# Optimization experiments

Measured on AMD Instinct MI355X. Metric: run time of the kernel, lower is better.

## Reference

```python
import jax, jax.numpy as jnp
import numpy as np

BS, N, HID = 16384, 16, 512  # batch, n coords (state dim = 2n), mlp hidden


def setup_inputs() -> dict:
    key = jax.random.key(0)
    ks = jax.random.split(key, 4)
    d = 2 * N
    x = jax.random.normal(ks[0], (BS, d), dtype=jnp.float32)
    # Lagrangian MLP: 2n -> HID -> HID -> 1 with softplus (smooth 2nd derivs)
    W1 = jax.random.normal(ks[1], (d, HID), dtype=jnp.float32) / np.sqrt(d)
    b1 = jnp.zeros((HID,), jnp.float32)
    W2 = jax.random.normal(ks[2], (HID, HID), dtype=jnp.float32) / np.sqrt(HID)
    b2 = jnp.zeros((HID,), jnp.float32)
    W3 = jax.random.normal(ks[3], (HID, 1), dtype=jnp.float32) / np.sqrt(HID)
    b3 = jnp.zeros((1,), jnp.float32)
    return {"x": x, "W1": W1, "b1": b1, "W2": W2, "b2": b2, "W3": W3, "b3": b3}


def reference(x, W1, b1, W2, b2, W3, b3):
    n = x.shape[1] // 2

    def lagrangian(qqd):  # qqd: [2n] -> scalar
        h = jax.nn.softplus(qqd @ W1 + b1)
        h = jax.nn.softplus(h @ W2 + b2)
        return jnp.sum(h @ W3 + b3)

    # batched first derivative (jacobian of scalar) and hessian; replaces the
    # per-sample python loop of torch.autograd.functional.jacobian/hessian
    jac = jax.vmap(jax.grad(lagrangian))(x)          # [bs, 2n]
    hess = jax.vmap(jax.hessian(lagrangian))(x)      # [bs, 2n, 2n]

    qd = x[:, n:]                                    # [bs, n]
    A = hess[:, n:, n:]                              # d2L/dqd dqd  [bs, n, n]
    B = hess[:, n:, :n]                              # d2L/dqd dq   [bs, n, n]
    rhs = jac[:, :n] - jnp.einsum('bij,bj->bi', B, qd)  # [bs, n]
    qdd = jnp.einsum('bij,bj->bi', jnp.linalg.pinv(A), rhs)  # [bs, n]
    return jnp.concatenate([qd, qdd], axis=1)        # [bs, 2n]
```

## Files before the change

### kernel.cpp

```cpp
#include <hip/hip_runtime.h>
#include <math.h>


#define NSWEEP 5
#define JAX_RCOND 1.9073486e-5

typedef unsigned int uint;
typedef unsigned short ushort;
typedef float f2 __attribute__((ext_vector_type(2)));
typedef float f4 __attribute__((ext_vector_type(4)));
typedef short bf16x8 __attribute__((ext_vector_type(8)));
typedef float f32x16 __attribute__((ext_vector_type(16)));
typedef uint uint2v __attribute__((ext_vector_type(2)));

#define OFF_R    0
#define R_FLOATS 6144
#define OFF_S1   (OFF_R + R_FLOATS)
#define OFF_H1   (OFF_S1+512)
#define OFF_G2   (OFF_H1+512)
#define OFF_D2   (OFF_G2+512)
#define OFF_U    (OFF_D2+512)
#define OFF_X    (OFF_U+512)
#define OFF_JAC  (OFF_X+32)
#define OFF_T1   (OFF_JAC+16)
#define OFF_T2   (OFF_T1+528)
#define OFF_AUG  (OFF_T2+528)
#define SMEM_FLOATS (OFF_AUG+272)
#define SMEM_BYTES  (SMEM_FLOATS*4)

#define SOLVE_WAVE_DBL 592
#define SOLVE_SMEM_BYTES (4*SOLVE_WAVE_DBL*8)

#define PACK_BYTES 524288

__device__ __forceinline__ ushort f2bf(float x) {
    uint u = __float_as_uint(x);
    return (ushort)((u + 0x7fffu + ((u >> 16) & 1u)) >> 16);
}
__device__ __forceinline__ float bf2f(ushort h) {
    return __uint_as_float(((uint)h) << 16);
}
__device__ __forceinline__ void split3(float x, ushort& h, ushort& m, ushort& l) {
    h = f2bf(x); float r1 = x - bf2f(h);
    m = f2bf(r1); float r2 = r1 - bf2f(m);
    l = f2bf(r2);
}

__device__ __forceinline__ void pairpq(int r, int m, int& p, int& q) {
    p = (m == 0) ? 0 : 1 + (m - 1 + r) % 15;
    q = 1 + (14 - m + r) % 15;
}

__device__ __forceinline__ void wave_fence() {
    __builtin_amdgcn_wave_barrier();
    __builtin_amdgcn_s_waitcnt(0);
    __builtin_amdgcn_wave_barrier();
}

__device__ __forceinline__ void jacobi_solve_wave(
    const float* __restrict__ gaug, double* __restrict__ ws,
    float* __restrict__ outp, int lane)
{
    double* Ad  = ws;
    double* Vd  = Ad + 272;
    double* c8  = Vd + 272;
    double* sn8 = c8 + 8;
    double* il  = sn8 + 8;
    double* yv  = il + 16;

    for (int idx = lane; idx < 272; idx += 64) {
        const int r = idx / 17, c = idx - r*17;
        double a = 0.0;
        if (c < 16) a = 0.5 * ((double)gaug[r*17 + c] + (double)gaug[c*17 + r]);
        Ad[idx] = a;
        Vd[idx] = (c < 16 && r == c) ? 1.0 : 0.0;
    }
    wave_fence();

    for (int sweep = 0; sweep < NSWEEP; ++sweep) {
        for (int rr = 0; rr < 15; ++rr) {
            if (lane < 8) {
                int p, q; pairpq(rr, lane, p, q);
                const double app = Ad[p*17 + p], aqq = Ad[q*17 + q], apq = Ad[p*17 + q];
                double cc = 1.0, ss = 0.0;
                if (apq != 0.0) {
                    const double tau = (aqq - app) / (2.0 * apq);
                    const double tt = ((tau >= 0.0) ? 1.0 : -1.0) / (fabs(tau) + sqrt(1.0 + tau*tau));
                    cc = 1.0 / sqrt(1.0 + tt*tt);
                    ss = tt * cc;
                }
                c8[lane] = cc; sn8[lane] = ss;
            }
            wave_fence();
            #pragma unroll
            for (int k = 0; k < 2; ++k) {
                const int id = lane + 64*k;
                const int m = id >> 4, j = id & 15;
                int p, q; pairpq(rr, m, p, q);
                const double cc = c8[m], ss = sn8[m];
                const double ap = Ad[p*17 + j], aq = Ad[q*17 + j];
                Ad[p*17 + j] = cc*ap - ss*aq;
                Ad[q*17 + j] = ss*ap + cc*aq;
            }
            #pragma unroll
            for (int k = 0; k < 2; ++k) {
                const int id = lane + 64*k;
                const int m = id >> 4, i = id & 15;
                int p, q; pairpq(rr, m, p, q);
                const double cc = c8[m], ss = sn8[m];
                const double vp = Vd[i*17 + p], vq = Vd[i*17 + q];
                Vd[i*17 + p] = cc*vp - ss*vq;
                Vd[i*17 + q] = ss*vp + cc*vq;
            }
            wave_fence();
            #pragma unroll
            for (int k = 0; k < 2; ++k) {
                const int id = lane + 64*k;
                const int m = id >> 4, i = id & 15;
                int p, q; pairpq(rr, m, p, q);
                const double cc = c8[m], ss = sn8[m];
                const double ap = Ad[i*17 + p], aq = Ad[i*17 + q];
                Ad[i*17 + p] = cc*ap - ss*aq;
                Ad[i*17 + q] = ss*ap + cc*aq;
            }
            wave_fence();
        }
    }

    if (lane == 0) {
        double mx = 0.0;
        #pragma unroll
        for (int i = 0; i < 16; ++i) mx = fmax(mx, fabs(Ad[i*17 + i]));
        const double cut = JAX_RCOND * mx;
        #pragma unroll
        for (int i = 0; i < 16; ++i) {
            const double l = Ad[i*17 + i];
            il[i] = (fabs(l) > cut) ? (1.0 / l) : 0.0;
        }
    }
    wave_fence();

    if (lane < 16) {
        double a = 0.0;
        #pragma unroll
        for (int r = 0; r < 16; ++r) a += Vd[r*17 + lane] * (double)gaug[r*17 + 16];
        yv[lane] = a;
    }
    wave_fence();

    if (lane < 16) {
        double a = 0.0;
        #pragma unroll
        for (int i = 0; i < 16; ++i) a += Vd[lane*17 + i] * (il[i] * yv[i]);
        outp[lane] = (float)a;
    }
}

extern "C" __global__ void w1_transpose(const float* __restrict__ W1,
                                        float* __restrict__ W1T) {
    const int t = blockIdx.x * 256 + threadIdx.x;
    W1T[t] = W1[(t & 31) * 512 + (t >> 5)];
}

extern "C" __global__ void w2_pack(const float* __restrict__ W2,
                                   uint* __restrict__ pHi,
                                   uint* __restrict__ pMid,
                                   uint* __restrict__ pLo) {
    const int tid = blockIdx.x * 256 + threadIdx.x;
    const int lane = tid & 63;
    const int k0 = ((tid >> 6) & 31) * 16 + (lane >> 5) * 8;
    const int n  = (tid >> 11) * 32 + (lane & 31);
    uint h[4], m[4], l[4];
    #pragma unroll
    for (int e2 = 0; e2 < 4; ++e2) {
        ushort h0, m0, l0, h1, m1, l1;
        split3(W2[(k0 + 2*e2    )*512 + n], h0, m0, l0);
        split3(W2[(k0 + 2*e2 + 1)*512 + n], h1, m1, l1);
        h[e2] = (uint)h0 | ((uint)h1 << 16);
        m[e2] = (uint)m0 | ((uint)m1 << 16);
        l[e2] = (uint)l0 | ((uint)l1 << 16);
    }
    #pragma unroll
    for (int e2 = 0; e2 < 4; ++e2) {
        pHi [tid*4 + e2] = h[e2];
        pMid[tid*4 + e2] = m[e2];
        pLo [tid*4 + e2] = l[e2];
    }
}

#define MFMA32(A, B, C) __builtin_amdgcn_mfma_f32_32x32x16_bf16((A), (B), (C), 0, 0, 0)

extern "C" __global__ __launch_bounds__(256, 4)
void lnn_kernel(const float* __restrict__ x,
                const float* __restrict__ W1,
                const float* __restrict__ W1T,
                const float* __restrict__ b1,
                const float* __restrict__ W2, const float* __restrict__ b2,
                const float* __restrict__ W3,
                float* __restrict__ out,
                float* __restrict__ aug_g,
                const uint* __restrict__ pHi,
                const uint* __restrict__ pMid,
                const uint* __restrict__ pLo,
                const int solveInMain)
{
    const int b = blockIdx.x;
    const int t = threadIdx.x;
    const int lane = t & 63;
    const int w = t >> 6;

    extern __shared__ float sm[];
    char*  A8    = (char*)sm;
    float* s_ws  = sm + OFF_R;
    char*  Mq8   = (char*)sm;
    float* s_s1  = sm + OFF_S1;
    float* s_h1  = sm + OFF_H1;
    float* s_g2  = sm + OFF_G2;
    float* s_d2  = sm + OFF_D2;
    float* s_u   = sm + OFF_U;
    float* s_x   = sm + OFF_X;
    float* s_jac = sm + OFF_JAC;
    float* s_T1  = sm + OFF_T1;
    float* s_T2  = sm + OFF_T2;
    float* s_aug = sm + OFF_AUG;

    if (t < 32) s_x[t] = x[b*32 + t];
    if (t < 16) out[b*32 + t] = x[b*32 + 16 + t];
    __syncthreads();

    #pragma unroll
    for (int rep = 0; rep < 2; ++rep) {
        const int j = t + rep*256;
        float z = b1[j];
        const f4* wt = (const f4*)(W1T + j*32);
        #pragma unroll
        for (int i4 = 0; i4 < 8; ++i4) {
            const f4 wv = wt[i4];
            z = fmaf(s_x[i4*4 + 0], wv.x, z);
            z = fmaf(s_x[i4*4 + 1], wv.y, z);
            z = fmaf(s_x[i4*4 + 2], wv.z, z);
            z = fmaf(s_x[i4*4 + 3], wv.w, z);
        }
        const float e = expf(-fabsf(z));
        const float s = (z >= 0.f) ? 1.f/(1.f+e) : e/(1.f+e);
        s_s1[j] = s;
        s_h1[j] = fmaxf(z, 0.f) + log1pf(e);
    }
    __syncthreads();

    {
        const int c = w*128 + lane*2;
        const f2 bz = *(const f2*)(b2 + c);
        float za0 = bz.x, za1 = bz.y;
        #pragma unroll 16
        for (int j = 0; j < 512; ++j) {
            const f2 wv = *(const f2*)(W2 + j*512 + c);
            const float h = s_h1[j];
            za0 = fmaf(h, wv.x, za0);
            za1 = fmaf(h, wv.y, za1);
        }
        const f2 w3v = *(const f2*)(W3 + c);
        const float e0 = expf(-fabsf(za0));
        const float sg0 = (za0 >= 0.f) ? 1.f/(1.f+e0) : e0/(1.f+e0);
        const float e1v = expf(-fabsf(za1));
        const float sg1 = (za1 >= 0.f) ? 1.f/(1.f+e1v) : e1v/(1.f+e1v);
        f2 g2v = { w3v.x * sg0, w3v.y * sg1 };
        f2 d2v = { w3v.x * sg0 * (1.f - sg0), w3v.y * sg1 * (1.f - sg1) };
        *(f2*)(s_g2 + c) = g2v;
        *(f2*)(s_d2 + c) = d2v;
    }
    __syncthreads();

    {
        float g2f[8];
        {
            const float4 ga = *(const float4*)(s_g2 + lane*8);
            const float4 gb = *(const float4*)(s_g2 + lane*8 + 4);
            g2f[0]=ga.x; g2f[1]=ga.y; g2f[2]=ga.z; g2f[3]=ga.w;
            g2f[4]=gb.x; g2f[5]=gb.y; g2f[6]=gb.z; g2f[7]=gb.w;
        }
        for (int jj = 0; jj < 32; ++jj) {
            float pr[4];
            #pragma unroll
            for (int s = 0; s < 4; ++s) {
                const int j = w*128 + jj + s*32;
                const float4 ra = *(const float4*)(W2 + j*512 + lane*8);
                const float4 rb = *(const float4*)(W2 + j*512 + lane*8 + 4);
                float p0 = ra.x*g2f[0];
                p0 = fmaf(ra.y, g2f[1], p0); p0 = fmaf(ra.z, g2f[2], p0); p0 = fmaf(ra.w, g2f[3], p0);
                p0 = fmaf(rb.x, g2f[4], p0); p0 = fmaf(rb.y, g2f[5], p0);
                p0 = fmaf(rb.z, g2f[6], p0); p0 = fmaf(rb.w, g2f[7], p0);
                pr[s] = p0;
            }
            #pragma unroll
            for (int off = 32; off >= 1; off >>= 1) {
                #pragma unroll
                for (int s = 0; s < 4; ++s) pr[s] += __shfl_xor(pr[s], off);
            }
            if (lane == 0) {
                #pragma unroll
                for (int s = 0; s < 4; ++s) s_u[w*128 + jj + s*32] = pr[s];
            }
        }
    }
    __syncthreads();

    #pragma unroll
    for (int rep = 0; rep < 2; ++rep) {
        const int j = t + rep*256;
        const float uj = s_u[j], s = s_s1[j];
        s_h1[j] = uj * (1.f - s) / s;
    }

    const int i5 = 16 + (t >> 4);
    const int c5 = 2 * (t & 15);

    {
        const f4* W1Tv4 = (const f4*)W1T;
        float jacp = 0.f, t1a = 0.f, t1b = 0.f;

        for (int q = 0; q < 4; ++q) {
            __syncthreads();
            #pragma unroll
            for (int r = 0; r < 4; ++r) {
                const int f = r*256 + t;
                f4 v = W1Tv4[q*1024 + f];
                const float s = s_s1[q*128 + (f >> 3)];
                v.x*=s; v.y*=s; v.z*=s; v.w*=s;
                ((f4*)s_ws)[f] = v;
            }
            __syncthreads();

            if (w == q) {
                const int i  = t & 15;
                const int jb = (lane >> 4) * 32;
                #pragma unroll 8
                for (int jj = 0; jj < 32; ++jj)
                    jacp = fmaf(s_ws[(jb+jj)*32 + i], s_u[q*128 + jb + jj], jacp);
            }

            #pragma unroll 4
            for (int jj = 0; jj < 128; ++jj) {
                const float e   = s_h1[q*128 + jj];
                const float wsi = s_ws[jj*32 + i5];
                const f2 wc = *(const f2*)(s_ws + jj*32 + c5);
                const float tt  = wsi * e;
                t1a = fmaf(tt, wc.x, t1a);
                t1b = fmaf(tt, wc.y, t1b);
            }
        }
        s_T1[(i5-16)*33 + c5]     = t1a;
        s_T1[(i5-16)*33 + c5 + 1] = t1b;
        s_g2[(t>>4)*16 + (t&15)]  = jacp;
    }
    __syncthreads();

    if (t < 16) {
        float p = 0.f;
        #pragma unroll
        for (int seg = 0; seg < 16; ++seg) p += s_g2[seg*16 + t];
        s_jac[t] = p;
    }

    float h0 = 0.f, h1v = 0.f;
    {
        const f4* W1v4 = (const f4*)W1;
        const f4* s1v4 = (const f4*)s_s1;
        const bf16x8* pHiV  = (const bf16x8*)pHi;
        const bf16x8* pMidV = (const bf16x8*)pMid;
        const bf16x8* pLoV  = (const bf16x8*)pLo;
        const int arow = lane & 31;
        const uint abase = (uint)arow * 256u;
        const uint aswz = (uint)(arow & 15);
        const f4* d2q = (const f4*)s_d2;
        const int rowadd = 4 * (lane >> 5);
        const int cl = lane & 31;
        const uint swi = (uint)((i5 >> 1) & 7);
        const uint swc = (uint)((c5 >> 1) & 7);
        char* MiB = Mq8 + i5*528;
        char* MaB = Mq8 + c5*528;
        char* MbB = Mq8 + (c5+1)*528;

        #pragma unroll 1
        for (int half = 0; half < 2; ++half) {
            f32x16 acc0{}, acc1{};
            const int NT0 = 2*half, NT1 = 2*half + 1;

            #pragma unroll 1
            for (int q = 0; q < 4; ++q) {
                __syncthreads();
                #pragma unroll
                for (int r = 0; r < 4; ++r) {
                    const int f = r*256 + t;
                    const int i = f >> 5, k4 = f & 31;
                    const f4 wv = W1v4[i*128 + q*32 + k4];
                    const f4 sv = s1v4[q*32 + k4];
                    ushort h[4], m[4], l[4];
                    split3(wv.x*sv.x, h[0], m[0], l[0]);
                    split3(wv.y*sv.y, h[1], m[1], l[1]);
                    split3(wv.z*sv.z, h[2], m[2], l[2]);
                    split3(wv.w*sv.w, h[3], m[3], l[3]);
                    const uint off = (uint)i*256u + (((uint)k4*8u) ^ (((uint)(i & 15)) << 4));
                    uint2v vh = { (uint)h[0] | ((uint)h[1]<<16), (uint)h[2] | ((uint)h[3]<<16) };
                    uint2v vm = { (uint)m[0] | ((uint)m[1]<<16), (uint)m[2] | ((uint)m[3]<<16) };
                    uint2v vl = { (uint)l[0] | ((uint)l[1]<<16), (uint)l[2] | ((uint)l[3]<<16) };
                    *(uint2v*)(A8 + off)         = vh;
                    *(uint2v*)(A8 + 8192 + off)  = vm;
                    *(uint2v*)(A8 + 16384 + off) = vl;
                }
                __syncthreads();

                #pragma unroll 2
                for (int ks8 = 0; ks8 < 8; ++ks8) {
                    const uint slot = (uint)(ks8*2 + (lane >> 5));
                    const uint aoff = abase + ((slot ^ aswz) << 4);
                    const bf16x8 aHi  = *(const bf16x8*)(A8 + aoff);
                    const bf16x8 aMid = *(const bf16x8*)(A8 + 8192 + aoff);
                    const bf16x8 aLo  = *(const bf16x8*)(A8 + 16384 + aoff);
                    const int pbase = (w*128 + q*8 + ks8)*64 + lane;
                    #define KSTEP(ACC, NT) { \
                        const bf16x8 bHi  = pHiV [pbase + (NT)*2048]; \
                        const bf16x8 bMid = pMidV[pbase + (NT)*2048]; \
                        const bf16x8 bLo  = pLoV [pbase + (NT)*2048]; \
                        ACC = MFMA32(aHi,  bHi,  ACC); \
                        ACC = MFMA32(aHi,  bMid, ACC); \
                        ACC = MFMA32(aMid, bHi,  ACC); \
                        ACC = MFMA32(aMid, bMid, ACC); \
                        ACC = MFMA32(aHi,  bLo,  ACC); \
                        ACC = MFMA32(aLo,  bHi,  ACC); }
                    KSTEP(acc0, NT0)
                    KSTEP(acc1, NT1)
                    #undef KSTEP
                }
            }
            __syncthreads();

            for (int p = 0; p < 4; ++p) {
                if (w == p) {
                    #define WRFRAG(ACC, NT) { \
                        _Pragma("unroll") \
                        for (int r = 0; r < 16; ++r) { \
                            const int row = (r & 3) + 8*(r >> 2) + rowadd; \
                            const int col = (NT)*32 + cl; \
                            const uint slot = ((uint)(col >> 2)) ^ ((uint)((row >> 1) & 7)); \
                            *(float*)(Mq8 + row*528 + (slot << 4) + ((col & 3) << 2)) = ACC[r]; \
                        } }
                    WRFRAG(acc0, NT0)
                    WRFRAG(acc1, NT1)
                    #undef WRFRAG
                }
                __syncthreads();
                for (int qq = half*16; qq < half*16 + 16; ++qq) {
                    const f4 d  = d2q[p*32 + qq];
                    const f4 mi = *(const f4*)(MiB + (((uint)qq ^ swi) << 4));
                    const f4 ma = *(const f4*)(MaB + (((uint)qq ^ swc) << 4));
                    const f4 mb = *(const f4*)(MbB + (((uint)qq ^ swc) << 4));
                    float tt;
                    tt = mi.x*d.x; h0 = fmaf(tt, ma.x, h0); h1v = fmaf(tt, mb.x, h1v);
                    tt = mi.y*d.y; h0 = fmaf(tt, ma.y, h0); h1v = fmaf(tt, mb.y, h1v);
                    tt = mi.z*d.z; h0 = fmaf(tt, ma.z, h0); h1v = fmaf(tt, mb.z, h1v);
                    tt = mi.w*d.w; h0 = fmaf(tt, ma.w, h0); h1v = fmaf(tt, mb.w, h1v);
                }
                __syncthreads();
            }
        }
        s_T2[(i5-16)*33 + c5]     = h0;
        s_T2[(i5-16)*33 + c5 + 1] = h1v;
    }
    __syncthreads();

    {
        const int r = t >> 4, c = t & 15;
        s_aug[r*17 + c] = s_T1[r*33 + 16 + c] + s_T2[r*33 + 16 + c];
    }
    if (t < 16) {
        float p = s_jac[t];
        #pragma unroll
        for (int c = 0; c < 16; ++c)
            p -= (s_T1[t*33 + c] + s_T2[t*33 + c]) * s_x[16 + c];
        s_aug[t*17 + 16] = p;
    }
    __syncthreads();

    if (!solveInMain) {
        aug_g[b*272 + t] = s_aug[t];
        if (t < 16) aug_g[b*272 + 256 + t] = s_aug[256 + t];
        return;
    }

    if (w != 0) return;
    jacobi_solve_wave(s_aug, (double*)sm, out + b*32 + 16, lane);
}

extern "C" __global__ __launch_bounds__(256, 8)
void lnn_solve(const float* __restrict__ aug_g, float* __restrict__ out)
{
    const int t = threadIdx.x;
    const int lane = t & 63;
    const int w = t >> 6;
    const int b = blockIdx.x * 4 + w;

    extern __shared__ double dsm[];
    jacobi_solve_wave(aug_g + b*272, dsm + w*SOLVE_WAVE_DBL, out + b*32 + 16, lane);
}

extern "C" void kernel_launch(void* const* d_in, const int* in_sizes, int n_in,
                              void* d_out, int out_size, void* d_ws, size_t ws_size,
                              hipStream_t stream) {
    const float* x  = (const float*)d_in[0];
    const float* W1 = (const float*)d_in[1];
    const float* b1 = (const float*)d_in[2];
    const float* W2 = (const float*)d_in[3];
    const float* b2 = (const float*)d_in[4];
    const float* W3 = (const float*)d_in[5];
    float* out = (float*)d_out;

    float* W1T = (float*)d_ws;
    uint*  pHi  = (uint*)((char*)d_ws + 65536);
    uint*  pMid = (uint*)((char*)d_ws + 65536 + PACK_BYTES);
    uint*  pLo  = (uint*)((char*)d_ws + 65536 + 2*PACK_BYTES);
    float* aug  = (float*)((char*)d_ws + 65536 + 3*PACK_BYTES);
    const int bs = in_sizes[0] / 32;

    const size_t need = 65536 + 3*(size_t)PACK_BYTES + (size_t)bs * 272 * 4;
    const int solveInMain = (ws_size < need) ? 1 : 0;

    hipFuncSetAttribute((const void*)lnn_kernel,
                        hipFuncAttributeMaxDynamicSharedMemorySize, SMEM_BYTES);
    w1_transpose<<<dim3(64), dim3(256), 0, stream>>>(W1, W1T);
    w2_pack<<<dim3(128), dim3(256), 0, stream>>>(W2, pHi, pMid, pLo);
    lnn_kernel<<<dim3(bs), dim3(256), SMEM_BYTES, stream>>>(
        x, W1, W1T, b1, W2, b2, W3, out, aug, pHi, pMid, pLo, solveInMain);
    if (!solveInMain)
        lnn_solve<<<dim3(bs/4), dim3(256), SOLVE_SMEM_BYTES, stream>>>(aug, out);
}
```

Measured before the change: 3.668 ms.

## Process two samples per block to reuse W1/W2 loads across samples

Measured after the change: 3.360 ms. 8.4% less time.

```diff
diff --git a/kernel.cpp b/kernel.cpp
--- a/kernel.cpp
+++ b/kernel.cpp
@@ -14,18 +14,18 @@
 typedef uint uint2v __attribute__((ext_vector_type(2)));
 
 #define OFF_R    0
-#define R_FLOATS 6144
-#define OFF_S1   (OFF_R + R_FLOATS)
-#define OFF_H1   (OFF_S1+512)
-#define OFF_G2   (OFF_H1+512)
-#define OFF_D2   (OFF_G2+512)
-#define OFF_U    (OFF_D2+512)
-#define OFF_X    (OFF_U+512)
-#define OFF_JAC  (OFF_X+32)
-#define OFF_T1   (OFF_JAC+16)
-#define OFF_T2   (OFF_T1+528)
-#define OFF_AUG  (OFF_T2+528)
-#define SMEM_FLOATS (OFF_AUG+272)
+#define R_FLOATS 12288
+#define OFF_S1   12288
+#define OFF_H1   13312
+#define OFF_G2   14336
+#define OFF_D2   15360
+#define OFF_U    16384
+#define OFF_X    17408
+#define OFF_JAC  17472
+#define OFF_T1   17504
+#define OFF_T2   18560
+#define OFF_AUG  19616
+#define SMEM_FLOATS 20160
 #define SMEM_BYTES  (SMEM_FLOATS*4)
 
 #define SOLVE_WAVE_DBL 592
@@ -190,7 +190,7 @@
 
 #define MFMA32(A, B, C) __builtin_amdgcn_mfma_f32_32x32x16_bf16((A), (B), (C), 0, 0, 0)
 
-extern "C" __global__ __launch_bounds__(256, 4)
+extern "C" __global__ __launch_bounds__(256, 2)
 void lnn_kernel(const float* __restrict__ x,
                 const float* __restrict__ W1,
                 const float* __restrict__ W1T,
@@ -204,7 +204,7 @@
                 const uint* __restrict__ pLo,
                 const int solveInMain)
 {
-    const int b = blockIdx.x;
+    const int b0 = blockIdx.x * 2;
     const int t = threadIdx.x;
     const int lane = t & 63;
     const int w = t >> 6;
@@ -224,92 +224,118 @@
     float* s_T2  = sm + OFF_T2;
     float* s_aug = sm + OFF_AUG;
 
-    if (t < 32) s_x[t] = x[b*32 + t];
-    if (t < 16) out[b*32 + t] = x[b*32 + 16 + t];
+    if (t < 64) s_x[t] = x[b0*32 + t];
+    if (t < 32) {
+        const int s = t >> 4, i = t & 15;
+        out[(b0+s)*32 + i] = x[(b0+s)*32 + 16 + i];
+    }
     __syncthreads();
 
     #pragma unroll
-    for (int rep = 0; rep < 2; ++rep) {
-        const int j = t + rep*256;
+    for (int rep = 0; rep < 4; ++rep) {
+        const int s = rep >> 1;
+        const int j = t + (rep & 1)*256;
         float z = b1[j];
         const f4* wt = (const f4*)(W1T + j*32);
+        const float* xs = s_x + s*32;
         #pragma unroll
         for (int i4 = 0; i4 < 8; ++i4) {
             const f4 wv = wt[i4];
-            z = fmaf(s_x[i4*4 + 0], wv.x, z);
-            z = fmaf(s_x[i4*4 + 1], wv.y, z);
-            z = fmaf(s_x[i4*4 + 2], wv.z, z);
-            z = fmaf(s_x[i4*4 + 3], wv.w, z);
+            z = fmaf(xs[i4*4 + 0], wv.x, z);
+            z = fmaf(xs[i4*4 + 1], wv.y, z);
+            z = fmaf(xs[i4*4 + 2], wv.z, z);
+            z = fmaf(xs[i4*4 + 3], wv.w, z);
         }
         const float e = expf(-fabsf(z));
-        const float s = (z >= 0.f) ? 1.f/(1.f+e) : e/(1.f+e);
-        s_s1[j] = s;
-        s_h1[j] = fmaxf(z, 0.f) + log1pf(e);
+        const float sg = (z >= 0.f) ? 1.f/(1.f+e) : e/(1.f+e);
+        s_s1[s*512 + j] = sg;
+        s_h1[s*512 + j] = fmaxf(z, 0.f) + log1pf(e);
     }
     __syncthreads();
 
     {
         const int c = w*128 + lane*2;
         const f2 bz = *(const f2*)(b2 + c);
-        float za0 = bz.x, za1 = bz.y;
-        #pragma unroll 16
+        float za[2][2] = { {bz.x, bz.y}, {bz.x, bz.y} };
+        #pragma unroll 8
         for (int j = 0; j < 512; ++j) {
             const f2 wv = *(const f2*)(W2 + j*512 + c);
-            const float h = s_h1[j];
-            za0 = fmaf(h, wv.x, za0);
-            za1 = fmaf(h, wv.y, za1);
+            const float h0 = s_h1[j];
+            const float h1 = s_h1[512 + j];
+            za[0][0] = fmaf(h0, wv.x, za[0][0]);
+            za[0][1] = fmaf(h0, wv.y, za[0][1]);
+            za[1][0] = fmaf(h1, wv.x, za[1][0]);
+            za[1][1] = fmaf(h1, wv.y, za[1][1]);
         }
         const f2 w3v = *(const f2*)(W3 + c);
-        const float e0 = expf(-fabsf(za0));
-        const float sg0 = (za0 >= 0.f) ? 1.f/(1.f+e0) : e0/(1.f+e0);
-        const float e1v = expf(-fabsf(za1));
-        const float sg1 = (za1 >= 0.f) ? 1.f/(1.f+e1v) : e1v/(1.f+e1v);
-        f2 g2v = { w3v.x * sg0, w3v.y * sg1 };
-        f2 d2v = { w3v.x * sg0 * (1.f - sg0), w3v.y * sg1 * (1.f - sg1) };
-        *(f2*)(s_g2 + c) = g2v;
-        *(f2*)(s_d2 + c) = d2v;
+        #pragma unroll
+        for (int s = 0; s < 2; ++s) {
+            const float e0 = expf(-fabsf(za[s][0]));
+            const float sg0 = (za[s][0] >= 0.f) ? 1.f/(1.f+e0) : e0/(1.f+e0);
+            const float e1v = expf(-fabsf(za[s][1]));
+            const float sg1 = (za[s][1] >= 0.f) ? 1.f/(1.f+e1v) : e1v/(1.f+e1v);
+            f2 g2v = { w3v.x * sg0, w3v.y * sg1 };
+            f2 d2v = { w3v.x * sg0 * (1.f - sg0), w3v.y * sg1 * (1.f - sg1) };
+            *(f2*)(s_g2 + s*512 + c) = g2v;
+            *(f2*)(s_d2 + s*512 + c) = d2v;
+        }
     }
     __syncthreads();
 
     {
-        float g2f[8];
+        float g2a[8], g2b[8];
         {
             const float4 ga = *(const float4*)(s_g2 + lane*8);
             const float4 gb = *(const float4*)(s_g2 + lane*8 + 4);
-            g2f[0]=ga.x; g2f[1]=ga.y; g2f[2]=ga.z; g2f[3]=ga.w;
-            g2f[4]=gb.x; g2f[5]=gb.y; g2f[6]=gb.z; g2f[7]=gb.w;
+            g2a[0]=ga.x; g2a[1]=ga.y; g2a[2]=ga.z; g2a[3]=ga.w;
+            g2a[4]=gb.x; g2a[5]=gb.y; g2a[6]=gb.z; g2a[7]=gb.w;
+            const float4 gc = *(const float4*)(s_g2 + 512 + lane*8);
+            const float4 gd = *(const float4*)(s_g2 + 512 + lane*8 + 4);
+            g2b[0]=gc.x; g2b[1]=gc.y; g2b[2]=gc.z; g2b[3]=gc.w;
+            g2b[4]=gd.x; g2b[5]=gd.y; g2b[6]=gd.z; g2b[7]=gd.w;
         }
         for (int jj = 0; jj < 32; ++jj) {
-            float pr[4];
+            float pr0[4], pr1[4];
             #pragma unroll
-            for (int s = 0; s < 4; ++s) {
-                const int j = w*128 + jj + s*32;
+            for (int s4 = 0; s4 < 4; ++s4) {
+                const int j = w*128 + jj + s4*32;
                 const float4 ra = *(const float4*)(W2 + j*512 + lane*8);
                 const float4 rb = *(const float4*)(W2 + j*512 + lane*8 + 4);
-                float p0 = ra.x*g2f[0];
-                p0 = fmaf(ra.y, g2f[1], p0); p0 = fmaf(ra.z, g2f[2], p0); p0 = fmaf(ra.w, g2f[3], p0);
-                p0 = fmaf(rb.x, g2f[4], p0); p0 = fmaf(rb.y, g2f[5], p0);
-                p0 = fmaf(rb.z, g2f[6], p0); p0 = fmaf(rb.w, g2f[7], p0);
-                pr[s] = p0;
+                float p0 = ra.x*g2a[0];
+                p0 = fmaf(ra.y, g2a[1], p0); p0 = fmaf(ra.z, g2a[2], p0); p0 = fmaf(ra.w, g2a[3], p0);
+                p0 = fmaf(rb.x, g2a[4], p0); p0 = fmaf(rb.y, g2a[5], p0);
+                p0 = fmaf(rb.z, g2a[6], p0); p0 = fmaf(rb.w, g2a[7], p0);
+                pr0[s4] = p0;
+                float p1 = ra.x*g2b[0];
+                p1 = fmaf(ra.y, g2b[1], p1); p1 = fmaf(ra.z, g2b[2], p1); p1 = fmaf(ra.w, g2b[3], p1);
+                p1 = fmaf(rb.x, g2b[4], p1); p1 = fmaf(rb.y, g2b[5], p1);
+                p1 = fmaf(rb.z, g2b[6], p1); p1 = fmaf(rb.w, g2b[7], p1);
+                pr1[s4] = p1;
             }
             #pragma unroll
             for (int off = 32; off >= 1; off >>= 1) {
                 #pragma unroll
-                for (int s = 0; s < 4; ++s) pr[s] += __shfl_xor(pr[s], off);
+                for (int s4 = 0; s4 < 4; ++s4) {
+                    pr0[s4] += __shfl_xor(pr0[s4], off);
+                    pr1[s4] += __shfl_xor(pr1[s4], off);
+                }
             }
             if (lane == 0) {
                 #pragma unroll
-                for (int s = 0; s < 4; ++s) s_u[w*128 + jj + s*32] = pr[s];
+                for (int s4 = 0; s4 < 4; ++s4) {
+                    s_u[w*128 + jj + s4*32]       = pr0[s4];
+                    s_u[512 + w*128 + jj + s4*32] = pr1[s4];
+                }
             }
         }
     }
     __syncthreads();
 
     #pragma unroll
-    for (int rep = 0; rep < 2; ++rep) {
-        const int j = t + rep*256;
-        const float uj = s_u[j], s = s_s1[j];
-        s_h1[j] = uj * (1.f - s) / s;
+    for (int rep = 0; rep < 4; ++rep) {
+        const int j = (rep >> 1)*512 + t + (rep & 1)*256;
+        const float uj = s_u[j], sv = s_s1[j];
+        s_h1[j] = uj * (1.f - sv) / sv;
     }
 
     const int i5 = 16 + (t >> 4);
@@ -317,52 +343,75 @@
 
     {
         const f4* W1Tv4 = (const f4*)W1T;
-        float jacp = 0.f, t1a = 0.f, t1b = 0.f;
+        float jacp[2] = {0.f, 0.f};
+        float t1a[2] = {0.f, 0.f}, t1b[2] = {0.f, 0.f};
 
         for (int q = 0; q < 4; ++q) {
             __syncthreads();
             #pragma unroll
             for (int r = 0; r < 4; ++r) {
                 const int f = r*256 + t;
-                f4 v = W1Tv4[q*1024 + f];
-                const float s = s_s1[q*128 + (f >> 3)];
-                v.x*=s; v.y*=s; v.z*=s; v.w*=s;
-                ((f4*)s_ws)[f] = v;
+                const f4 wv = W1Tv4[q*1024 + f];
+                #pragma unroll
+                for (int s = 0; s < 2; ++s) {
+                    const float sv = s_s1[s*512 + q*128 + (f >> 3)];
+                    f4 v = wv;
+                    v.x*=sv; v.y*=sv; v.z*=sv; v.w*=sv;
+                    ((f4*)(s_ws + s*4096))[f] = v;
+                }
             }
             __syncthreads();
 
             if (w == q) {
                 const int i  = t & 15;
                 const int jb = (lane >> 4) * 32;
-                #pragma unroll 8
-                for (int jj = 0; jj < 32; ++jj)
-                    jacp = fmaf(s_ws[(jb+jj)*32 + i], s_u[q*128 + jb + jj], jacp);
-            }
-
-            #pragma unroll 4
-            for (int jj = 0; jj < 128; ++jj) {
-                const float e   = s_h1[q*128 + jj];
-                const float wsi = s_ws[jj*32 + i5];
-                const f2 wc = *(const f2*)(s_ws + jj*32 + c5);
-                const float tt  = wsi * e;
-                t1a = fmaf(tt, wc.x, t1a);
-                t1b = fmaf(tt, wc.y, t1b);
-            }
-        }
-        s_T1[(i5-16)*33 + c5]     = t1a;
-        s_T1[(i5-16)*33 + c5 + 1] = t1b;
-        s_g2[(t>>4)*16 + (t&15)]  = jacp;
+                #pragma unroll
+                for (int s = 0; s < 2; ++s) {
+                    const float* wsp = s_ws + s*4096;
+                    const float* up  = s_u + s*512 + q*128;
+                    float jp = jacp[s];
+                    #pragma unroll 8
+                    for (int jj = 0; jj < 32; ++jj)
+                        jp = fmaf(wsp[(jb+jj)*32 + i], up[jb + jj], jp);
+                    jacp[s] = jp;
+                }
+            }
+
+            #pragma unroll
+            for (int s = 0; s < 2; ++s) {
+                const float* wsp = s_ws + s*4096;
+                const float* ep  = s_h1 + s*512 + q*128;
+                float a = t1a[s], bv = t1b[s];
+                #pragma unroll 4
+                for (int jj = 0; jj < 128; ++jj) {
+                    const float e   = ep[jj];
+                    const float wsi = wsp[jj*32 + i5];
+                    const f2 wc = *(const f2*)(wsp + jj*32 + c5);
+                    const float tt  = wsi * e;
+                    a  = fmaf(tt, wc.x, a);
+                    bv = fmaf(tt, wc.y, bv);
+                }
+                t1a[s] = a; t1b[s] = bv;
+            }
+        }
+        #pragma unroll
+        for (int s = 0; s < 2; ++s) {
+            s_T1[s*528 + (i5-16)*33 + c5]     = t1a[s];
+            s_T1[s*528 + (i5-16)*33 + c5 + 1] = t1b[s];
+            s_g2[s*512 + (t>>4)*16 + (t&15)]  = jacp[s];
+        }
     }
     __syncthreads();
 
-    if (t < 16) {
+    if (t < 32) {
+        const int s = t >> 4, i = t & 15;
         float p = 0.f;
         #pragma unroll
-        for (int seg = 0; seg < 16; ++seg) p += s_g2[seg*16 + t];
-        s_jac[t] = p;
-    }
-
-    float h0 = 0.f, h1v = 0.f;
+        for (int seg = 0; seg < 16; ++seg) p += s_g2[s*512 + seg*16 + i];
+        s_jac[s*16 + i] = p;
+    }
+
+    float h0acc[2] = {0.f, 0.f}, h1acc[2] = {0.f, 0.f};
     {
         const f4* W1v4 = (const f4*)W1;
         const f4* s1v4 = (const f4*)s_s1;
@@ -372,18 +421,14 @@
         const int arow = lane & 31;
         const uint abase = (uint)arow * 256u;
         const uint aswz = (uint)(arow & 15);
-        const f4* d2q = (const f4*)s_d2;
         const int rowadd = 4 * (lane >> 5);
         const int cl = lane & 31;
         const uint swi = (uint)((i5 >> 1) & 7);
         const uint swc = (uint)((c5 >> 1) & 7);
-        char* MiB = Mq8 + i5*528;
-        char* MaB = Mq8 + c5*528;
-        char* MbB = Mq8 + (c5+1)*528;
 
         #pragma unroll 1
         for (int half = 0; half < 2; ++half) {
-            f32x16 acc0{}, acc1{};
+            f32x16 acc00{}, acc01{}, acc10{}, acc11{};
             const int NT0 = 2*half, NT1 = 2*half + 1;
 
             #pragma unroll 1
@@ -394,19 +439,23 @@
                     const int f = r*256 + t;
                     const int i = f >> 5, k4 = f & 31;
                     const f4 wv = W1v4[i*128 + q*32 + k4];
-                    const f4 sv = s1v4[q*32 + k4];
-                    ushort h[4], m[4], l[4];
-                    split3(wv.x*sv.x, h[0], m[0], l[0]);
-                    split3(wv.y*sv.y, h[1], m[1], l[1]);
-                    split3(wv.z*sv.z, h[2], m[2], l[2]);
-                    split3(wv.w*sv.w, h[3], m[3], l[3]);
                     const uint off = (uint)i*256u + (((uint)k4*8u) ^ (((uint)(i & 15)) << 4));
-                    uint2v vh = { (uint)h[0] | ((uint)h[1]<<16), (uint)h[2] | ((uint)h[3]<<16) };
-                    uint2v vm = { (uint)m[0] | ((uint)m[1]<<16), (uint)m[2] | ((uint)m[3]<<16) };
-                    uint2v vl = { (uint)l[0] | ((uint)l[1]<<16), (uint)l[2] | ((uint)l[3]<<16) };
-                    *(uint2v*)(A8 + off)         = vh;
-                    *(uint2v*)(A8 + 8192 + off)  = vm;
-                    *(uint2v*)(A8 + 16384 + off) = vl;
+                    #pragma unroll
+                    for (int s = 0; s < 2; ++s) {
+                        const f4 sv = s1v4[s*128 + q*32 + k4];
+                        ushort h[4], m[4], l[4];
+                        split3(wv.x*sv.x, h[0], m[0], l[0]);
+                        split3(wv.y*sv.y, h[1], m[1], l[1]);
+                        split3(wv.z*sv.z, h[2], m[2], l[2]);
+                        split3(wv.w*sv.w, h[3], m[3], l[3]);
+                        uint2v vh = { (uint)h[0] | ((uint)h[1]<<16), (uint)h[2] | ((uint)h[3]<<16) };
+                        uint2v vm = { (uint)m[0] | ((uint)m[1]<<16), (uint)m[2] | ((uint)m[3]<<16) };
+                        uint2v vl = { (uint)l[0] | ((uint)l[1]<<16), (uint)l[2] | ((uint)l[3]<<16) };
+                        char* base = A8 + s*24576;
+                        *(uint2v*)(base + off)         = vh;
+                        *(uint2v*)(base + 8192 + off)  = vm;
+                        *(uint2v*)(base + 16384 + off) = vl;
+                    }
                 }
                 __syncthreads();
 
@@ -414,22 +463,31 @@
                 for (int ks8 = 0; ks8 < 8; ++ks8) {
                     const uint slot = (uint)(ks8*2 + (lane >> 5));
                     const uint aoff = abase + ((slot ^ aswz) << 4);
-                    const bf16x8 aHi  = *(const bf16x8*)(A8 + aoff);
-                    const bf16x8 aMid = *(const bf16x8*)(A8 + 8192 + aoff);
-                    const bf16x8 aLo  = *(const bf16x8*)(A8 + 16384 + aoff);
+                    const bf16x8 aHi0  = *(const bf16x8*)(A8 + aoff);
+                    const bf16x8 aMid0 = *(const bf16x8*)(A8 + 8192 + aoff);
+                    const bf16x8 aLo0  = *(const bf16x8*)(A8 + 16384 + aoff);
+                    const bf16x8 aHi1  = *(const bf16x8*)(A8 + 24576 + aoff);
+                    const bf16x8 aMid1 = *(const bf16x8*)(A8 + 24576 + 8192 + aoff);
+                    const bf16x8 aLo1  = *(const bf16x8*)(A8 + 24576 + 16384 + aoff);
                     const int pbase = (w*128 + q*8 + ks8)*64 + lane;
-                    #define KSTEP(ACC, NT) { \
+                    #define KSTEP(A0, A1, NT) { \
                         const bf16x8 bHi  = pHiV [pbase + (NT)*2048]; \
                         const bf16x8 bMid = pMidV[pbase + (NT)*2048]; \
                         const bf16x8 bLo  = pLoV [pbase + (NT)*2048]; \
-                        ACC = MFMA32(aHi,  bHi,  ACC); \
-                        ACC = MFMA32(aHi,  bMid, ACC); \
-                        ACC = MFMA32(aMid, bHi,  ACC); \
-                        ACC = MFMA32(aMid, bMid, ACC); \
-                        ACC = MFMA32(aHi,  bLo,  ACC); \
-                        ACC = MFMA32(aLo,  bHi,  ACC); }
-                    KSTEP(acc0, NT0)
-                    KSTEP(acc1, NT1)
+                        A0 = MFMA32(aHi0,  bHi,  A0); \
+                        A0 = MFMA32(aHi0,  bMid, A0); \
+                        A0 = MFMA32(aMid0, bHi,  A0); \
+                        A0 = MFMA32(aMid0, bMid, A0); \
+                        A0 = MFMA32(aHi0,  bLo,  A0); \
+                        A0 = MFMA32(aLo0,  bHi,  A0); \
+                        A1 = MFMA32(aHi1,  bHi,  A1); \
+                        A1 = MFMA32(aHi1,  bMid, A1); \
+                        A1 = MFMA32(aMid1, bHi,  A1); \
+                        A1 = MFMA32(aMid1, bMid, A1); \
+                        A1 = MFMA32(aHi1,  bLo,  A1); \
+                        A1 = MFMA32(aLo1,  bHi,  A1); }
+                    KSTEP(acc00, acc10, NT0)
+                    KSTEP(acc01, acc11, NT1)
                     #undef KSTEP
                 }
             }
@@ -437,59 +495,78 @@
 
             for (int p = 0; p < 4; ++p) {
                 if (w == p) {
-                    #define WRFRAG(ACC, NT) { \
+                    #define WRFRAG(ACC, SOFF, NT) { \
                         _Pragma("unroll") \
                         for (int r = 0; r < 16; ++r) { \
                             const int row = (r & 3) + 8*(r >> 2) + rowadd; \
                             const int col = (NT)*32 + cl; \
                             const uint slot = ((uint)(col >> 2)) ^ ((uint)((row >> 1) & 7)); \
-                            *(float*)(Mq8 + row*528 + (slot << 4) + ((col & 3) << 2)) = ACC[r]; \
+                            *(float*)(Mq8 + (SOFF) + row*528 + (slot << 4) + ((col & 3) << 2)) = ACC[r]; \
                         } }
-                    WRFRAG(acc0, NT0)
-                    WRFRAG(acc1, NT1)
+                    WRFRAG(acc00, 0, NT0)
+                    WRFRAG(acc01, 0, NT1)
+                    WRFRAG(acc10, 16896, NT0)
+                    WRFRAG(acc11, 16896, NT1)
                     #undef WRFRAG
                 }
                 __syncthreads();
-                for (int qq = half*16; qq < half*16 + 16; ++qq) {
-                    const f4 d  = d2q[p*32 + qq];
-                    const f4 mi = *(const f4*)(MiB + (((uint)qq ^ swi) << 4));
-                    const f4 ma = *(const f4*)(MaB + (((uint)qq ^ swc) << 4));
-                    const f4 mb = *(const f4*)(MbB + (((uint)qq ^ swc) << 4));
-                    float tt;
-                    tt = mi.x*d.x; h0 = fmaf(tt, ma.x, h0); h1v = fmaf(tt, mb.x, h1v);
-                    tt = mi.y*d.y; h0 = fmaf(tt, ma.y, h0); h1v = fmaf(tt, mb.y, h1v);
-                    tt = mi.z*d.z; h0 = fmaf(tt, ma.z, h0); h1v = fmaf(tt, mb.z, h1v);
-                    tt = mi.w*d.w; h0 = fmaf(tt, ma.w, h0); h1v = fmaf(tt, mb.w, h1v);
+                #pragma unroll
+                for (int s = 0; s < 2; ++s) {
+                    const f4* d2q = (const f4*)(s_d2 + s*512);
+                    const char* MiB = Mq8 + s*16896 + i5*528;
+                    const char* MaB = Mq8 + s*16896 + c5*528;
+                    const char* MbB = Mq8 + s*16896 + (c5+1)*528;
+                    float h0 = h0acc[s], h1v = h1acc[s];
+                    for (int qq = half*16; qq < half*16 + 16; ++qq) {
+                        const f4 d  = d2q[p*32 + qq];
+                        const f4 mi = *(const f4*)(MiB + (((uint)qq ^ swi) << 4));
+                        const f4 ma = *(const f4*)(MaB + (((uint)qq ^ swc) << 4));
+                        const f4 mb = *(const f4*)(MbB + (((uint)qq ^ swc) << 4));
+                        float tt;
+                        tt = mi.x*d.x; h0 = fmaf(tt, ma.x, h0); h1v = fmaf(tt, mb.x, h1v);
+                        tt = mi.y*d.y; h0 = fmaf(tt, ma.y, h0); h1v = fmaf(tt, mb.y, h1v);
+                        tt = mi.z*d.z; h0 = fmaf(tt, ma.z, h0); h1v = fmaf(tt, mb.z, h1v);
+                        tt = mi.w*d.w; h0 = fmaf(tt, ma.w, h0); h1v = fmaf(tt, mb.w, h1v);
+                    }
+                    h0acc[s] = h0; h1acc[s] = h1v;
                 }
                 __syncthreads();
             }
         }
-        s_T2[(i5-16)*33 + c5]     = h0;
-        s_T2[(i5-16)*33 + c5 + 1] = h1v;
+        #pragma unroll
+        for (int s = 0; s < 2; ++s) {
+            s_T2[s*528 + (i5-16)*33 + c5]     = h0acc[s];
+            s_T2[s*528 + (i5-16)*33 + c5 + 1] = h1acc[s];
+        }
     }
     __syncthreads();
 
     {
         const int r = t >> 4, c = t & 15;
-        s_aug[r*17 + c] = s_T1[r*33 + 16 + c] + s_T2[r*33 + 16 + c];
-    }
-    if (t < 16) {
-        float p = s_jac[t];
+        #pragma unroll
+        for (int s = 0; s < 2; ++s)
+            s_aug[s*272 + r*17 + c] = s_T1[s*528 + r*33 + 16 + c] + s_T2[s*528 + r*33 + 16 + c];
+    }
+    if (t < 32) {
+        const int s = t >> 4, i = t & 15;
+        float p = s_jac[s*16 + i];
         #pragma unroll
         for (int c = 0; c < 16; ++c)
-            p -= (s_T1[t*33 + c] + s_T2[t*33 + c]) * s_x[16 + c];
-        s_aug[t*17 + 16] = p;
+            p -= (s_T1[s*528 + i*33 + c] + s_T2[s*528 + i*33 + c]) * s_x[s*32 + 16 + c];
+        s_aug[s*272 + i*17 + 16] = p;
     }
     __syncthreads();
 
     if (!solveInMain) {
-        aug_g[b*272 + t] = s_aug[t];
-        if (t < 16) aug_g[b*272 + 256 + t] = s_aug[256 + t];
+        aug_g[b0*272 + t]       = s_aug[t];
+        aug_g[b0*272 + 256 + t] = s_aug[256 + t];
+        if (t < 32) aug_g[b0*272 + 512 + t] = s_aug[512 + t];
         return;
     }
 
-    if (w != 0) return;
-    jacobi_solve_wave(s_aug, (double*)sm, out + b*32 + 16, lane);
+    if (w >= 2) return;
+    jacobi_solve_wave(s_aug + w*272, (double*)sm + w*SOLVE_WAVE_DBL,
+                      out + (b0+w)*32 + 16, lane);
 }
 
 extern "C" __global__ __launch_bounds__(256, 8)
@@ -529,7 +606,7 @@
                         hipFuncAttributeMaxDynamicSharedMemorySize, SMEM_BYTES);
     w1_transpose<<<dim3(64), dim3(256), 0, stream>>>(W1, W1T);
     w2_pack<<<dim3(128), dim3(256), 0, stream>>>(W2, pHi, pMid, pLo);
-    lnn_kernel<<<dim3(bs), dim3(256), SMEM_BYTES, stream>>>(
+    lnn_kernel<<<dim3(bs/2), dim3(256), SMEM_BYTES, stream>>>(
         x, W1, W1T, b1, W2, b2, W3, out, aug, pHi, pMid, pLo, solveInMain);
     if (!solveInMain)
         lnn_solve<<<dim3(bs/4), dim3(256), SOLVE_SMEM_BYTES, stream>>>(aug, out);
```
